# Optimization experiments

Measured on AMD Instinct MI355X. Metric: run time of the kernel, lower is better.

Reference implementation:

```python
import jax, jax.numpy as jnp
import numpy as np

B, S, D, E, K = 4, 2048, 2048, 64, 2

def setup_inputs() -> dict:
    key = jax.random.key(0)
    k1, k2, k3, k4 = jax.random.split(key, 4)
    x = jax.random.normal(k1, (B, S, D), dtype=jnp.float32)
    W = jax.random.normal(k2, (E, D), dtype=jnp.float32) * 0.02  # gate_linear.weight
    noise_weight = jax.random.normal(k3, (E,), dtype=jnp.float32) * 0.02
    noise = jax.random.normal(k4, (B, S, E), dtype=jnp.float32)  # torch.randn_like(logits), noisy_std=1.0
    return {"x": x, "W": W, "noise_weight": noise_weight, "noise": noise, "k": K}

def reference(x, W, noise_weight, noise, k):
    # logits = x @ W.T  -> [B, S, E]
    logits = jnp.einsum('bsd,ed->bse', x, W)
    # noise injection: randn * noisy_std(=1.0) * noise_weight (per-expert scale)
    logits_noisy = logits + noise * noise_weight
    # top-k over experts
    top_vals, top_idx = jax.lax.top_k(logits_noisy, k)  # [B, S, k]
    # softmax over a tensor that is -inf everywhere except the top-k slots is
    # exactly: zeros everywhere, softmax(top_vals) scattered into the top-k slots.
    probs = jax.nn.softmax(top_vals, axis=-1)  # [B, S, k]
    n_tok = B * S
    rows = jnp.arange(n_tok)[:, None]  # [n_tok, 1]
    gated = jnp.zeros((n_tok, E), dtype=logits.dtype)
    gated = gated.at[rows, top_idx.reshape(n_tok, k)].set(probs.reshape(n_tok, k))
    gated = gated.reshape(B, S, E)
    return gated, top_idx, top_vals
```

## Files before the change

### kernel.cpp

```cpp
#include <hip/hip_runtime.h>
#include <math.h>

#define NTOK 8192
#define DDIM 2048
#define NEXP 64
#define MT   16
#define BK   64
#define KHALF 1024
#define NCH  (KHALF / BK)
#define XSTR 72
#define CSTR 66

typedef _Float16 f16x8 __attribute__((ext_vector_type(8)));
typedef _Float16 f16x4 __attribute__((ext_vector_type(4)));
typedef float    f32x4 __attribute__((ext_vector_type(4)));

#define GATED_SZ (NTOK * NEXP)
#define IDX_OFF  GATED_SZ
#define VALS_OFF (GATED_SZ + NTOK * 2)

#define NKSTEP (DDIM / 32)
#define NTILE  (NEXP / 16)
#define BFRAG_HALVES ((size_t)NKSTEP * NTILE * 64 * 8)

__global__ void pack_b_kernel(const float* __restrict__ W,
                              _Float16* __restrict__ Bh,
                              _Float16* __restrict__ Bl)
{
    const int tid  = blockIdx.x * blockDim.x + threadIdx.x;
    const int lane = tid & 63;
    const int fid  = tid >> 6;
    const int ks   = fid >> 2;
    const int nt   = fid & 3;
    const int e    = nt * 16 + (lane & 15);
    const int k    = ks * 32 + (lane >> 4) * 8;
    const float* src = W + (size_t)e * DDIM + k;

    f16x8 hi, lo;
#pragma unroll
    for (int j = 0; j < 8; ++j) {
        const float v = src[j];
        const _Float16 h = (_Float16)v;
        hi[j] = h;
        lo[j] = (_Float16)((v - (float)h) * 4096.f);
    }
    *(f16x8*)(Bh + (size_t)tid * 8) = hi;
    *(f16x8*)(Bl + (size_t)tid * 8) = lo;
}

__global__ __launch_bounds__(512, 4) void gate_kernel(
    const float* __restrict__ x,
    const _Float16* __restrict__ Bh,
    const _Float16* __restrict__ Bl,
    const float* __restrict__ noise_w,
    const float* __restrict__ noise,
    float* __restrict__ out)
{
    __shared__ _Float16 xh[2][MT * XSTR];
    __shared__ _Float16 xl[2][MT * XSTR];
    __shared__ float    cbuf[2][MT * CSTR];

    const int tid  = threadIdx.x;
    const int lane = tid & 63;
    const int w    = __builtin_amdgcn_readfirstlane(tid >> 6);
    const int s    = w >> 2;
    const int nt   = w & 3;
    const int tokBase = blockIdx.x * MT;

    const int hid  = tid & 255;
    const int srow = hid >> 4;
    const int scol = (hid & 15) * 4;
    const float* xsrc = x + (size_t)(tokBase + srow) * DDIM + s * KHALF + scol;

    const int q = lane >> 4;
    const int m = lane & 15;
    const int abase = m * XSTR + q * 8;

    f32x4 acc_hh = {0.f, 0.f, 0.f, 0.f};
    f32x4 acc_lo = {0.f, 0.f, 0.f, 0.f};

    float4 stage = *(const float4*)xsrc;

    for (int c = 0; c < NCH; ++c) {
        __syncthreads();
        {
            f16x4 h4, l4;
            const float vv[4] = {stage.x, stage.y, stage.z, stage.w};
#pragma unroll
            for (int j = 0; j < 4; ++j) {
                const _Float16 h = (_Float16)vv[j];
                h4[j] = h;
                l4[j] = (_Float16)((vv[j] - (float)h) * 4096.f);
            }
            *(f16x4*)&xh[s][srow * XSTR + scol] = h4;
            *(f16x4*)&xl[s][srow * XSTR + scol] = l4;
        }
        if (c + 1 < NCH)
            stage = *(const float4*)(xsrc + (size_t)(c + 1) * BK);
        __syncthreads();

        const size_t ks0 = (size_t)s * 32 + 2 * c;
        const f16x8 bh0 = *(const f16x8*)(Bh + (((ks0    ) * 4 + nt) * 64 + lane) * 8);
        const f16x8 bh1 = *(const f16x8*)(Bh + (((ks0 + 1) * 4 + nt) * 64 + lane) * 8);
        const f16x8 bl0 = *(const f16x8*)(Bl + (((ks0    ) * 4 + nt) * 64 + lane) * 8);
        const f16x8 bl1 = *(const f16x8*)(Bl + (((ks0 + 1) * 4 + nt) * 64 + lane) * 8);

        const f16x8 ah0 = *(const f16x8*)&xh[s][abase];
        const f16x8 ah1 = *(const f16x8*)&xh[s][abase + 32];
        const f16x8 al0 = *(const f16x8*)&xl[s][abase];
        const f16x8 al1 = *(const f16x8*)&xl[s][abase + 32];

        acc_hh = __builtin_amdgcn_mfma_f32_16x16x32_f16(ah0, bh0, acc_hh, 0, 0, 0);
        acc_hh = __builtin_amdgcn_mfma_f32_16x16x32_f16(ah1, bh1, acc_hh, 0, 0, 0);
        acc_lo = __builtin_amdgcn_mfma_f32_16x16x32_f16(ah0, bl0, acc_lo, 0, 0, 0);
        acc_lo = __builtin_amdgcn_mfma_f32_16x16x32_f16(al0, bh0, acc_lo, 0, 0, 0);
        acc_lo = __builtin_amdgcn_mfma_f32_16x16x32_f16(ah1, bl1, acc_lo, 0, 0, 0);
        acc_lo = __builtin_amdgcn_mfma_f32_16x16x32_f16(al1, bh1, acc_lo, 0, 0, 0);
    }

    {
        const int e = nt * 16 + m;
#pragma unroll
        for (int r = 0; r < 4; ++r) {
            const int t = q * 4 + r;
            cbuf[s][t * CSTR + e] = acc_hh[r] + acc_lo[r] * (1.f / 4096.f);
        }
    }
    __syncthreads();

    const float nwv = noise_w[lane];
#pragma unroll
    for (int i = 0; i < 2; ++i) {
        const int t   = w * 2 + i;
        const int tok = tokBase + t;
        const int e   = lane;

        float v = cbuf[0][t * CSTR + e] + cbuf[1][t * CSTR + e]
                + noise[(size_t)tok * NEXP + e] * nwv;

        float m1 = v; int i1 = e;
#pragma unroll
        for (int sh = 32; sh > 0; sh >>= 1) {
            float ov = __shfl_xor(m1, sh, 64);
            int   oi = __shfl_xor(i1, sh, 64);
            if (ov > m1 || (ov == m1 && oi < i1)) { m1 = ov; i1 = oi; }
        }
        float vm = (e == i1) ? -INFINITY : v;
        float m2 = vm; int i2 = e;
#pragma unroll
        for (int sh = 32; sh > 0; sh >>= 1) {
            float ov = __shfl_xor(m2, sh, 64);
            int   oi = __shfl_xor(i2, sh, 64);
            if (ov > m2 || (ov == m2 && oi < i2)) { m2 = ov; i2 = oi; }
        }

        const float e2  = expf(m2 - m1);
        const float inv = 1.f / (1.f + e2);
        const float p1  = inv;
        const float p2  = e2 * inv;

        float gval = 0.f;
        if (e == i1) gval = p1;
        else if (e == i2) gval = p2;
        out[(size_t)tok * NEXP + e] = gval;

        if (lane == 0) {
            out[IDX_OFF  + tok * 2 + 0] = (float)i1;
            out[IDX_OFF  + tok * 2 + 1] = (float)i2;
            out[VALS_OFF + tok * 2 + 0] = m1;
            out[VALS_OFF + tok * 2 + 1] = m2;
        }
    }
}

extern "C" void kernel_launch(void* const* d_in, const int* in_sizes, int n_in,
                              void* d_out, int out_size, void* d_ws, size_t ws_size,
                              hipStream_t stream) {
    const float* x      = (const float*)d_in[0];
    const float* W      = (const float*)d_in[1];
    const float* nw     = (const float*)d_in[2];
    const float* noise  = (const float*)d_in[3];
    float* out = (float*)d_out;

    _Float16* Bh = (_Float16*)d_ws;
    _Float16* Bl = Bh + BFRAG_HALVES;

    hipLaunchKernelGGL(pack_b_kernel, dim3(64), dim3(256), 0, stream, W, Bh, Bl);

    hipLaunchKernelGGL(gate_kernel, dim3(NTOK / MT), dim3(512), 0, stream,
                       x, Bh, Bl, nw, noise, out);
}
```

Baseline: 116.8 us.

## Double-buffer shared x tiles and prefetch B fragments one chunk ahead

```diff
diff --git a/kernel.cpp b/kernel.cpp
--- a/kernel.cpp
+++ b/kernel.cpp
@@ -48,6 +48,8 @@
     *(f16x8*)(Bl + (size_t)tid * 8) = lo;
 }
 
+#define BFRAG(base, ks) (*(const f16x8*)((base) + ((((size_t)(ks)) * 4 + nt) * 64 + lane) * 8))
+
 __global__ __launch_bounds__(512, 4) void gate_kernel(
     const float* __restrict__ x,
     const _Float16* __restrict__ Bh,
@@ -56,8 +58,8 @@
     const float* __restrict__ noise,
     float* __restrict__ out)
 {
-    __shared__ _Float16 xh[2][MT * XSTR];
-    __shared__ _Float16 xl[2][MT * XSTR];
+    __shared__ _Float16 xh[2][2][MT * XSTR];
+    __shared__ _Float16 xl[2][2][MT * XSTR];
     __shared__ float    cbuf[2][MT * CSTR];
 
     const int tid  = threadIdx.x;
@@ -79,43 +81,58 @@
     f32x4 acc_hh = {0.f, 0.f, 0.f, 0.f};
     f32x4 acc_lo = {0.f, 0.f, 0.f, 0.f};
 
-    float4 stage = *(const float4*)xsrc;
-
+    float4 xsreg[2];
+    xsreg[0] = *(const float4*)xsrc;
+    xsreg[1] = *(const float4*)(xsrc + BK);
+
+    const int ksb = s * 32;
+    f16x8 bh0c = BFRAG(Bh, ksb + 0);
+    f16x8 bh1c = BFRAG(Bh, ksb + 1);
+    f16x8 bl0c = BFRAG(Bl, ksb + 0);
+    f16x8 bl1c = BFRAG(Bl, ksb + 1);
+
+#pragma unroll
     for (int c = 0; c < NCH; ++c) {
-        __syncthreads();
+        const int p = c & 1;
+
         {
+            const float4 sv = xsreg[p];
+            const float vv[4] = {sv.x, sv.y, sv.z, sv.w};
             f16x4 h4, l4;
-            const float vv[4] = {stage.x, stage.y, stage.z, stage.w};
 #pragma unroll
             for (int j = 0; j < 4; ++j) {
                 const _Float16 h = (_Float16)vv[j];
                 h4[j] = h;
                 l4[j] = (_Float16)((vv[j] - (float)h) * 4096.f);
             }
-            *(f16x4*)&xh[s][srow * XSTR + scol] = h4;
-            *(f16x4*)&xl[s][srow * XSTR + scol] = l4;
-        }
-        if (c + 1 < NCH)
-            stage = *(const float4*)(xsrc + (size_t)(c + 1) * BK);
+            *(f16x4*)&xh[s][p][srow * XSTR + scol] = h4;
+            *(f16x4*)&xl[s][p][srow * XSTR + scol] = l4;
+        }
+
+        if (c + 2 < NCH)
+            xsreg[p] = *(const float4*)(xsrc + (size_t)(c + 2) * BK);
+
+        const int cn = (c + 1 < NCH) ? (c + 1) : 0;
+        f16x8 bh0n = BFRAG(Bh, ksb + 2 * cn);
+        f16x8 bh1n = BFRAG(Bh, ksb + 2 * cn + 1);
+        f16x8 bl0n = BFRAG(Bl, ksb + 2 * cn);
+        f16x8 bl1n = BFRAG(Bl, ksb + 2 * cn + 1);
+
         __syncthreads();
 
-        const size_t ks0 = (size_t)s * 32 + 2 * c;
-        const f16x8 bh0 = *(const f16x8*)(Bh + (((ks0    ) * 4 + nt) * 64 + lane) * 8);
-        const f16x8 bh1 = *(const f16x8*)(Bh + (((ks0 + 1) * 4 + nt) * 64 + lane) * 8);
-        const f16x8 bl0 = *(const f16x8*)(Bl + (((ks0    ) * 4 + nt) * 64 + lane) * 8);
-        const f16x8 bl1 = *(const f16x8*)(Bl + (((ks0 + 1) * 4 + nt) * 64 + lane) * 8);
-
-        const f16x8 ah0 = *(const f16x8*)&xh[s][abase];
-        const f16x8 ah1 = *(const f16x8*)&xh[s][abase + 32];
-        const f16x8 al0 = *(const f16x8*)&xl[s][abase];
-        const f16x8 al1 = *(const f16x8*)&xl[s][abase + 32];
-
-        acc_hh = __builtin_amdgcn_mfma_f32_16x16x32_f16(ah0, bh0, acc_hh, 0, 0, 0);
-        acc_hh = __builtin_amdgcn_mfma_f32_16x16x32_f16(ah1, bh1, acc_hh, 0, 0, 0);
-        acc_lo = __builtin_amdgcn_mfma_f32_16x16x32_f16(ah0, bl0, acc_lo, 0, 0, 0);
-        acc_lo = __builtin_amdgcn_mfma_f32_16x16x32_f16(al0, bh0, acc_lo, 0, 0, 0);
-        acc_lo = __builtin_amdgcn_mfma_f32_16x16x32_f16(ah1, bl1, acc_lo, 0, 0, 0);
-        acc_lo = __builtin_amdgcn_mfma_f32_16x16x32_f16(al1, bh1, acc_lo, 0, 0, 0);
+        const f16x8 ah0 = *(const f16x8*)&xh[s][p][abase];
+        const f16x8 ah1 = *(const f16x8*)&xh[s][p][abase + 32];
+        const f16x8 al0 = *(const f16x8*)&xl[s][p][abase];
+        const f16x8 al1 = *(const f16x8*)&xl[s][p][abase + 32];
+
+        acc_hh = __builtin_amdgcn_mfma_f32_16x16x32_f16(ah0, bh0c, acc_hh, 0, 0, 0);
+        acc_hh = __builtin_amdgcn_mfma_f32_16x16x32_f16(ah1, bh1c, acc_hh, 0, 0, 0);
+        acc_lo = __builtin_amdgcn_mfma_f32_16x16x32_f16(ah0, bl0c, acc_lo, 0, 0, 0);
+        acc_lo = __builtin_amdgcn_mfma_f32_16x16x32_f16(al0, bh0c, acc_lo, 0, 0, 0);
+        acc_lo = __builtin_amdgcn_mfma_f32_16x16x32_f16(ah1, bl1c, acc_lo, 0, 0, 0);
+        acc_lo = __builtin_amdgcn_mfma_f32_16x16x32_f16(al1, bh1c, acc_lo, 0, 0, 0);
+
+        bh0c = bh0n; bh1c = bh1n; bl0c = bl0n; bl1c = bl1n;
     }
 
     {
```

After: 116.8 us. No clear change (-0.0%).

## Use wider K chunks with double-buffered LDS and single sync per step

Applied to the files above, without the earlier changes.

```diff
diff --git a/kernel.cpp b/kernel.cpp
--- a/kernel.cpp
+++ b/kernel.cpp
@@ -5,14 +5,12 @@
 #define DDIM 2048
 #define NEXP 64
 #define MT   16
-#define BK   64
-#define KHALF 1024
-#define NCH  (KHALF / BK)
-#define XSTR 72
+#define BK   256
+#define NCH  (DDIM / BK)
+#define XSTR 264
 #define CSTR 66
 
 typedef _Float16 f16x8 __attribute__((ext_vector_type(8)));
-typedef _Float16 f16x4 __attribute__((ext_vector_type(4)));
 typedef float    f32x4 __attribute__((ext_vector_type(4)));
 
 #define GATED_SZ (NTOK * NEXP)
@@ -48,6 +46,8 @@
     *(f16x8*)(Bl + (size_t)tid * 8) = lo;
 }
 
+#define BFRAG(base, ks) (*(const f16x8*)((base) + ((((size_t)(ks)) * 4 + nt) * 64 + lane) * 8))
+
 __global__ __launch_bounds__(512, 4) void gate_kernel(
     const float* __restrict__ x,
     const _Float16* __restrict__ Bh,
@@ -63,59 +63,59 @@
     const int tid  = threadIdx.x;
     const int lane = tid & 63;
     const int w    = __builtin_amdgcn_readfirstlane(tid >> 6);
-    const int s    = w >> 2;
+    const int h    = w >> 2;
     const int nt   = w & 3;
     const int tokBase = blockIdx.x * MT;
 
-    const int hid  = tid & 255;
-    const int srow = hid >> 4;
-    const int scol = (hid & 15) * 4;
-    const float* xsrc = x + (size_t)(tokBase + srow) * DDIM + s * KHALF + scol;
+    const int srow = tid >> 5;
+    const int scol = tid & 31;
+    const float* xsrc = x + (size_t)(tokBase + srow) * DDIM + scol * 8;
 
     const int q = lane >> 4;
     const int m = lane & 15;
-    const int abase = m * XSTR + q * 8;
+    const int abase = m * XSTR + h * (BK / 2) + q * 8;
 
     f32x4 acc_hh = {0.f, 0.f, 0.f, 0.f};
     f32x4 acc_lo = {0.f, 0.f, 0.f, 0.f};
 
-    float4 stage = *(const float4*)xsrc;
+    float4 st0 = *(const float4*)(xsrc);
+    float4 st1 = *(const float4*)(xsrc + 4);
 
     for (int c = 0; c < NCH; ++c) {
-        __syncthreads();
+        const int p = c & 1;
+
         {
-            f16x4 h4, l4;
-            const float vv[4] = {stage.x, stage.y, stage.z, stage.w};
+            f16x8 h8, l8;
+            const float vv[8] = {st0.x, st0.y, st0.z, st0.w,
+                                 st1.x, st1.y, st1.z, st1.w};
 #pragma unroll
-            for (int j = 0; j < 4; ++j) {
-                const _Float16 h = (_Float16)vv[j];
-                h4[j] = h;
-                l4[j] = (_Float16)((vv[j] - (float)h) * 4096.f);
+            for (int j = 0; j < 8; ++j) {
+                const _Float16 hh = (_Float16)vv[j];
+                h8[j] = hh;
+                l8[j] = (_Float16)((vv[j] - (float)hh) * 4096.f);
             }
-            *(f16x4*)&xh[s][srow * XSTR + scol] = h4;
-            *(f16x4*)&xl[s][srow * XSTR + scol] = l4;
+            *(f16x8*)&xh[p][srow * XSTR + scol * 8] = h8;
+            *(f16x8*)&xl[p][srow * XSTR + scol * 8] = l8;
         }
-        if (c + 1 < NCH)
-            stage = *(const float4*)(xsrc + (size_t)(c + 1) * BK);
+
+        if (c + 1 < NCH) {
+            st0 = *(const float4*)(xsrc + (size_t)(c + 1) * BK);
+            st1 = *(const float4*)(xsrc + (size_t)(c + 1) * BK + 4);
+        }
+
         __syncthreads();
 
-        const size_t ks0 = (size_t)s * 32 + 2 * c;
-        const f16x8 bh0 = *(const f16x8*)(Bh + (((ks0    ) * 4 + nt) * 64 + lane) * 8);
-        const f16x8 bh1 = *(const f16x8*)(Bh + (((ks0 + 1) * 4 + nt) * 64 + lane) * 8);
-        const f16x8 bl0 = *(const f16x8*)(Bl + (((ks0    ) * 4 + nt) * 64 + lane) * 8);
-        const f16x8 bl1 = *(const f16x8*)(Bl + (((ks0 + 1) * 4 + nt) * 64 + lane) * 8);
-
-        const f16x8 ah0 = *(const f16x8*)&xh[s][abase];
-        const f16x8 ah1 = *(const f16x8*)&xh[s][abase + 32];
-        const f16x8 al0 = *(const f16x8*)&xl[s][abase];
-        const f16x8 al1 = *(const f16x8*)&xl[s][abase + 32];
-
-        acc_hh = __builtin_amdgcn_mfma_f32_16x16x32_f16(ah0, bh0, acc_hh, 0, 0, 0);
-        acc_hh = __builtin_amdgcn_mfma_f32_16x16x32_f16(ah1, bh1, acc_hh, 0, 0, 0);
-        acc_lo = __builtin_amdgcn_mfma_f32_16x16x32_f16(ah0, bl0, acc_lo, 0, 0, 0);
-        acc_lo = __builtin_amdgcn_mfma_f32_16x16x32_f16(al0, bh0, acc_lo, 0, 0, 0);
-        acc_lo = __builtin_amdgcn_mfma_f32_16x16x32_f16(ah1, bl1, acc_lo, 0, 0, 0);
-        acc_lo = __builtin_amdgcn_mfma_f32_16x16x32_f16(al1, bh1, acc_lo, 0, 0, 0);
+        const int ksb = c * 8 + h * 4;
+#pragma unroll
+        for (int stp = 0; stp < 4; ++stp) {
+            const f16x8 bh = BFRAG(Bh, ksb + stp);
+            const f16x8 bl = BFRAG(Bl, ksb + stp);
+            const f16x8 ah = *(const f16x8*)&xh[p][abase + stp * 32];
+            const f16x8 al = *(const f16x8*)&xl[p][abase + stp * 32];
+            acc_hh = __builtin_amdgcn_mfma_f32_16x16x32_f16(ah, bh, acc_hh, 0, 0, 0);
+            acc_lo = __builtin_amdgcn_mfma_f32_16x16x32_f16(ah, bl, acc_lo, 0, 0, 0);
+            acc_lo = __builtin_amdgcn_mfma_f32_16x16x32_f16(al, bh, acc_lo, 0, 0, 0);
+        }
     }
 
     {
@@ -123,7 +123,7 @@
 #pragma unroll
         for (int r = 0; r < 4; ++r) {
             const int t = q * 4 + r;
-            cbuf[s][t * CSTR + e] = acc_hh[r] + acc_lo[r] * (1.f / 4096.f);
+            cbuf[h][t * CSTR + e] = acc_hh[r] + acc_lo[r] * (1.f / 4096.f);
         }
     }
     __syncthreads();
```

Result: faster. 112.5 us (-3.7%).
